# Optimization experiments

Hardware: AMD Instinct MI355X
Metric: run time of the kernel (lower is better)

## Reference

```python
import jax, jax.numpy as jnp
import numpy as np

ALPHA, BETA, GAMMA = 2.0, 2.0, 1.0
EPS = 1e-8  # torch F.cosine_similarity eps
B, T, D = 64, 1024, 256


def setup_inputs() -> dict:
    key = jax.random.key(0)
    k1, k2, k3 = jax.random.split(key, 3)
    f_v = jax.random.normal(k1, (B, T, D), dtype=jnp.float32)
    f_a = jax.random.normal(k2, (B, T, D), dtype=jnp.float32)
    labels = jax.random.randint(k3, (B,), 0, 2, dtype=jnp.int64)
    return {"f_v": f_v, "f_a": f_a, "labels": labels}


def _normalize(x):
    n = jnp.sqrt(jnp.sum(x * x, axis=-1, keepdims=True))
    return x / jnp.maximum(n, EPS)


def reference(f_v, f_a, labels):
    b, t, _ = f_v.shape
    vn = _normalize(f_v)  # [B,T,D]
    an = _normalize(f_a)  # [B,T,D]

    # --- per-timestep aligned-pair term ---
    cos_bt = jnp.sum(vn * an, axis=-1)  # [B,T] cosine sim
    d_bt = 1.0 - cos_bt                  # cosine distance
    pos_mask = (labels == 0).astype(f_v.dtype)[:, None]  # [B,1]
    neg_mask = 1.0 - pos_mask
    loss_pos = ALPHA * jnp.sum(d_bt * pos_mask)
    cnt_pos = jnp.sum(pos_mask) * t
    loss_neg = BETA * jnp.sum((1.0 - d_bt) * neg_mask)  # (1-d) == cos
    cnt_neg = jnp.sum(neg_mask) * t

    # --- cross-sample term: for i != j, (1 - mean_t d_ij) = mean_t cos(v_i_t, a_j_t) ---
    cross_cos = jnp.einsum('itd,jtd->ij', vn, an) / t  # [B,B] mean over T
    offdiag = 1.0 - jnp.eye(b, dtype=f_v.dtype)
    loss_neg = loss_neg + GAMMA * jnp.sum(cross_cos * offdiag)
    cnt_neg = cnt_neg + b * (b - 1)

    loss = jnp.where(cnt_pos > 0, loss_pos / jnp.maximum(cnt_pos, 1.0), 0.0)
    loss = loss + jnp.where(cnt_neg > 0, loss_neg / jnp.maximum(cnt_neg, 1.0), 0.0)
    return loss
```

## Files before the change

### kernel.cpp

```cpp
#include <hip/hip_runtime.h>

constexpr int Bn = 64;
constexpr int Tn = 1024;
constexpr int Dn = 256;

constexpr int TPB    = 256;
constexpr int NBLK   = 512;
constexpr int TPERB  = Tn / NBLK;
constexpr int KC     = 64;
constexpr int NCHUNK = Dn / KC;
constexpr int PITCH  = KC + 4;

__device__ __forceinline__ float dot4(const float4& a, const float4& b) {
    return a.x * b.x + a.y * b.y + a.z * b.z + a.w * b.w;
}

__global__ __launch_bounds__(TPB, 2)
void cmfm_main(const float* __restrict__ fv, const float* __restrict__ fa,
               const int* __restrict__ labels, float* __restrict__ acc) {
    __shared__ __align__(16) float Vs[Bn][PITCH];
    __shared__ __align__(16) float As[KC][PITCH];
    __shared__ float rvs[Bn];
    __shared__ float ras[Bn];
    __shared__ float wred[3][TPB / 64];

    const int tid = threadIdx.x;
    const int row = tid >> 2;
    const int q   = tid & 3;
    const int tx  = tid & 15;
    const int ty  = tid >> 4;
    const int i0  = ty * 4;
    const int j0  = tx * 4;

    const int lab = labels[row];

    const float4* __restrict__ fv4 = reinterpret_cast<const float4*>(fv);
    const float4* __restrict__ fa4 = reinterpret_cast<const float4*>(fa);

    float C[4][4] = {};
    float pos_acc = 0.f, neg_acc = 0.f;

    for (int tt = 0; tt < TPERB; ++tt) {
        const int t = blockIdx.x * TPERB + tt;
        const size_t base = ((size_t)row * Tn + t) * (Dn / 4);

        float S[4][4] = {};
        float sqv = 0.f, sqa = 0.f, dva = 0.f;

        for (int c = 0; c < NCHUNK; ++c) {
            const size_t f4base = base + (size_t)c * (KC / 4);
            float4 v4[4], a4[4];
            #pragma unroll
            for (int k = 0; k < 4; ++k) {
                const int f4i = q + 4 * k;
                v4[k] = fv4[f4base + f4i];
                a4[k] = fa4[f4base + f4i];
            }
            #pragma unroll
            for (int k = 0; k < 4; ++k) {
                sqv += dot4(v4[k], v4[k]);
                sqa += dot4(a4[k], a4[k]);
                dva += dot4(v4[k], a4[k]);
                const int d = (q + 4 * k) * 4;
                *reinterpret_cast<float4*>(&Vs[row][d]) = v4[k];
                As[d + 0][row] = a4[k].x;
                As[d + 1][row] = a4[k].y;
                As[d + 2][row] = a4[k].z;
                As[d + 3][row] = a4[k].w;
            }
            __syncthreads();

            #pragma unroll
            for (int d4 = 0; d4 < KC / 4; ++d4) {
                float va[4][4], ab[4][4];
                #pragma unroll
                for (int r = 0; r < 4; ++r) {
                    float4 v = *reinterpret_cast<const float4*>(&Vs[i0 + r][d4 * 4]);
                    va[r][0] = v.x; va[r][1] = v.y; va[r][2] = v.z; va[r][3] = v.w;
                }
                #pragma unroll
                for (int m = 0; m < 4; ++m) {
                    float4 a = *reinterpret_cast<const float4*>(&As[d4 * 4 + m][j0]);
                    ab[m][0] = a.x; ab[m][1] = a.y; ab[m][2] = a.z; ab[m][3] = a.w;
                }
                #pragma unroll
                for (int dd = 0; dd < 4; ++dd)
                    #pragma unroll
                    for (int r = 0; r < 4; ++r)
                        #pragma unroll
                        for (int s = 0; s < 4; ++s)
                            S[r][s] = fmaf(va[r][dd], ab[dd][s], S[r][s]);
            }
            __syncthreads();
        }

        sqv += __shfl_xor(sqv, 1); sqv += __shfl_xor(sqv, 2);
        sqa += __shfl_xor(sqa, 1); sqa += __shfl_xor(sqa, 2);
        dva += __shfl_xor(dva, 1); dva += __shfl_xor(dva, 2);
        const float rv = 1.f / fmaxf(sqrtf(sqv), 1e-8f);
        const float ra = 1.f / fmaxf(sqrtf(sqa), 1e-8f);
        if (q == 0) {
            rvs[row] = rv;
            ras[row] = ra;
            const float cosd = dva * rv * ra;
            if (lab == 0) pos_acc += 1.f - cosd;
            else          neg_acc += cosd;
        }
        __syncthreads();

        float rvv[4], raa[4];
        #pragma unroll
        for (int r = 0; r < 4; ++r) rvv[r] = rvs[i0 + r];
        #pragma unroll
        for (int s = 0; s < 4; ++s) raa[s] = ras[j0 + s];
        #pragma unroll
        for (int r = 0; r < 4; ++r)
            #pragma unroll
            for (int s = 0; s < 4; ++s)
                C[r][s] = fmaf(rvv[r] * raa[s], S[r][s], C[r][s]);
        __syncthreads();
    }

    float od = 0.f;
    #pragma unroll
    for (int r = 0; r < 4; ++r)
        #pragma unroll
        for (int s = 0; s < 4; ++s) od += C[r][s];
    if (ty == tx) {
        #pragma unroll
        for (int r = 0; r < 4; ++r) od -= C[r][r];
    }

    #pragma unroll
    for (int off = 1; off < 64; off <<= 1) {
        pos_acc += __shfl_xor(pos_acc, off);
        neg_acc += __shfl_xor(neg_acc, off);
        od      += __shfl_xor(od, off);
    }
    const int wave = tid >> 6;
    const int lane = tid & 63;
    if (lane == 0) {
        wred[0][wave] = pos_acc;
        wred[1][wave] = neg_acc;
        wred[2][wave] = od;
    }
    __syncthreads();
    if (tid == 0) {
        float p = 0.f, n = 0.f, o = 0.f;
        #pragma unroll
        for (int w = 0; w < TPB / 64; ++w) { p += wred[0][w]; n += wred[1][w]; o += wred[2][w]; }
        atomicAdd(&acc[0], p);
        atomicAdd(&acc[1], n);
        atomicAdd(&acc[2], o);
    }
}

__global__ void cmfm_final(const int* __restrict__ labels, const float* __restrict__ acc,
                           float* __restrict__ out) {
    if (threadIdx.x == 0) {
        int npos = 0;
        for (int i = 0; i < Bn; ++i) npos += (labels[i] == 0);
        const float pos_sum   = acc[0];
        const float neg_sum   = acc[1];
        const float cross_sum = acc[2];

        const float cnt_pos = (float)npos * (float)Tn;
        const float cnt_neg = (float)(Bn - npos) * (float)Tn + (float)Bn * (float)(Bn - 1);

        float loss = 0.f;
        if (npos > 0) loss += 2.0f * pos_sum / cnt_pos;
        loss += (2.0f * neg_sum + 1.0f * cross_sum / (float)Tn) / cnt_neg;
        out[0] = loss;
    }
}

extern "C" void kernel_launch(void* const* d_in, const int* in_sizes, int n_in,
                              void* d_out, int out_size, void* d_ws, size_t ws_size,
                              hipStream_t stream) {
    const float* fv     = (const float*)d_in[0];
    const float* fa     = (const float*)d_in[1];
    const int*   labels = (const int*)d_in[2];
    float* acc = (float*)d_ws;
    float* out = (float*)d_out;

    hipMemsetAsync(acc, 0, 3 * sizeof(float), stream);
    cmfm_main<<<NBLK, TPB, 0, stream>>>(fv, fa, labels, acc);
    cmfm_final<<<1, 64, 0, stream>>>(labels, acc, out);
}
```

Baseline: 171.0 us.

## Replace cross Gram matrix with sum-of-normalized-vectors dot product identity

Computes the off-diagonal cross-cosine sum as the dot of summed normalized v and a vectors per timestep minus the diagonal, eliminating the per-timestep 64x64 matrix product. Blocks now handle one timestep each and accumulate per-dimension column sums in shared memory over row groups. This turns a compute-bound kernel into a bandwidth-bound one, at the cost of possible float cancellation when subtracting the diagonal from the full sum.

```diff
diff --git a/kernel.cpp b/kernel.cpp
--- a/kernel.cpp
+++ b/kernel.cpp
@@ -4,154 +4,108 @@
 constexpr int Tn = 1024;
 constexpr int Dn = 256;
 
-constexpr int TPB    = 256;
-constexpr int NBLK   = 512;
-constexpr int TPERB  = Tn / NBLK;
-constexpr int KC     = 64;
-constexpr int NCHUNK = Dn / KC;
-constexpr int PITCH  = KC + 4;
+constexpr int TPB   = 256;
+constexpr int RG    = 16;
+constexpr int NG    = Bn / RG;
+constexpr int PITCH = Dn + 4;
 
 __device__ __forceinline__ float dot4(const float4& a, const float4& b) {
     return a.x * b.x + a.y * b.y + a.z * b.z + a.w * b.w;
 }
 
-__global__ __launch_bounds__(TPB, 2)
+__global__ __launch_bounds__(TPB, 4)
 void cmfm_main(const float* __restrict__ fv, const float* __restrict__ fa,
                const int* __restrict__ labels, float* __restrict__ acc) {
-    __shared__ __align__(16) float Vs[Bn][PITCH];
-    __shared__ __align__(16) float As[KC][PITCH];
-    __shared__ float rvs[Bn];
-    __shared__ float ras[Bn];
-    __shared__ float wred[3][TPB / 64];
+    __shared__ __align__(16) float Vs[RG][PITCH];
+    __shared__ __align__(16) float As[RG][PITCH];
+    __shared__ float rvl[RG];
+    __shared__ float ral[RG];
+    __shared__ float wred[4][TPB / 64];
 
     const int tid = threadIdx.x;
-    const int row = tid >> 2;
-    const int q   = tid & 3;
-    const int tx  = tid & 15;
-    const int ty  = tid >> 4;
-    const int i0  = ty * 4;
-    const int j0  = tx * 4;
-
-    const int lab = labels[row];
+    const int r16 = tid >> 4;
+    const int dp  = tid & 15;
+    const int t   = blockIdx.x;
 
     const float4* __restrict__ fv4 = reinterpret_cast<const float4*>(fv);
     const float4* __restrict__ fa4 = reinterpret_cast<const float4*>(fa);
 
-    float C[4][4] = {};
-    float pos_acc = 0.f, neg_acc = 0.f;
+    float pos_acc = 0.f, neg_acc = 0.f, diag_acc = 0.f;
+    float svd = 0.f, sad = 0.f;
 
-    for (int tt = 0; tt < TPERB; ++tt) {
-        const int t = blockIdx.x * TPERB + tt;
+    for (int g = 0; g < NG; ++g) {
+        const int row = g * RG + r16;
         const size_t base = ((size_t)row * Tn + t) * (Dn / 4);
 
-        float S[4][4] = {};
+        float4 v4[4], a4[4];
+        #pragma unroll
+        for (int k = 0; k < 4; ++k) {
+            v4[k] = fv4[base + dp + 16 * k];
+            a4[k] = fa4[base + dp + 16 * k];
+        }
         float sqv = 0.f, sqa = 0.f, dva = 0.f;
-
-        for (int c = 0; c < NCHUNK; ++c) {
-            const size_t f4base = base + (size_t)c * (KC / 4);
-            float4 v4[4], a4[4];
-            #pragma unroll
-            for (int k = 0; k < 4; ++k) {
-                const int f4i = q + 4 * k;
-                v4[k] = fv4[f4base + f4i];
-                a4[k] = fa4[f4base + f4i];
-            }
-            #pragma unroll
-            for (int k = 0; k < 4; ++k) {
-                sqv += dot4(v4[k], v4[k]);
-                sqa += dot4(a4[k], a4[k]);
-                dva += dot4(v4[k], a4[k]);
-                const int d = (q + 4 * k) * 4;
-                *reinterpret_cast<float4*>(&Vs[row][d]) = v4[k];
-                As[d + 0][row] = a4[k].x;
-                As[d + 1][row] = a4[k].y;
-                As[d + 2][row] = a4[k].z;
-                As[d + 3][row] = a4[k].w;
-            }
-            __syncthreads();
-
-            #pragma unroll
-            for (int d4 = 0; d4 < KC / 4; ++d4) {
-                float va[4][4], ab[4][4];
-                #pragma unroll
-                for (int r = 0; r < 4; ++r) {
-                    float4 v = *reinterpret_cast<const float4*>(&Vs[i0 + r][d4 * 4]);
-                    va[r][0] = v.x; va[r][1] = v.y; va[r][2] = v.z; va[r][3] = v.w;
-                }
-                #pragma unroll
-                for (int m = 0; m < 4; ++m) {
-                    float4 a = *reinterpret_cast<const float4*>(&As[d4 * 4 + m][j0]);
-                    ab[m][0] = a.x; ab[m][1] = a.y; ab[m][2] = a.z; ab[m][3] = a.w;
-                }
-                #pragma unroll
-                for (int dd = 0; dd < 4; ++dd)
-                    #pragma unroll
-                    for (int r = 0; r < 4; ++r)
-                        #pragma unroll
-                        for (int s = 0; s < 4; ++s)
-                            S[r][s] = fmaf(va[r][dd], ab[dd][s], S[r][s]);
-            }
-            __syncthreads();
+        #pragma unroll
+        for (int k = 0; k < 4; ++k) {
+            sqv += dot4(v4[k], v4[k]);
+            sqa += dot4(a4[k], a4[k]);
+            dva += dot4(v4[k], a4[k]);
+            const int d = (dp + 16 * k) * 4;
+            *reinterpret_cast<float4*>(&Vs[r16][d]) = v4[k];
+            *reinterpret_cast<float4*>(&As[r16][d]) = a4[k];
         }
-
-        sqv += __shfl_xor(sqv, 1); sqv += __shfl_xor(sqv, 2);
-        sqa += __shfl_xor(sqa, 1); sqa += __shfl_xor(sqa, 2);
-        dva += __shfl_xor(dva, 1); dva += __shfl_xor(dva, 2);
-        const float rv = 1.f / fmaxf(sqrtf(sqv), 1e-8f);
-        const float ra = 1.f / fmaxf(sqrtf(sqa), 1e-8f);
-        if (q == 0) {
-            rvs[row] = rv;
-            ras[row] = ra;
+        #pragma unroll
+        for (int off = 1; off < 16; off <<= 1) {
+            sqv += __shfl_xor(sqv, off);
+            sqa += __shfl_xor(sqa, off);
+            dva += __shfl_xor(dva, off);
+        }
+        if (dp == 0) {
+            const float rv = 1.f / fmaxf(sqrtf(sqv), 1e-8f);
+            const float ra = 1.f / fmaxf(sqrtf(sqa), 1e-8f);
+            rvl[r16] = rv;
+            ral[r16] = ra;
             const float cosd = dva * rv * ra;
-            if (lab == 0) pos_acc += 1.f - cosd;
-            else          neg_acc += cosd;
+            diag_acc += cosd;
+            if (labels[row] == 0) pos_acc += 1.f - cosd;
+            else                  neg_acc += cosd;
         }
         __syncthreads();
 
-        float rvv[4], raa[4];
         #pragma unroll
-        for (int r = 0; r < 4; ++r) rvv[r] = rvs[i0 + r];
-        #pragma unroll
-        for (int s = 0; s < 4; ++s) raa[s] = ras[j0 + s];
-        #pragma unroll
-        for (int r = 0; r < 4; ++r)
-            #pragma unroll
-            for (int s = 0; s < 4; ++s)
-                C[r][s] = fmaf(rvv[r] * raa[s], S[r][s], C[r][s]);
+        for (int i = 0; i < RG; ++i) {
+            svd = fmaf(rvl[i], Vs[i][tid], svd);
+            sad = fmaf(ral[i], As[i][tid], sad);
+        }
         __syncthreads();
     }
 
-    float od = 0.f;
-    #pragma unroll
-    for (int r = 0; r < 4; ++r)
-        #pragma unroll
-        for (int s = 0; s < 4; ++s) od += C[r][s];
-    if (ty == tx) {
-        #pragma unroll
-        for (int r = 0; r < 4; ++r) od -= C[r][r];
-    }
-
+    float dotp = svd * sad;
     #pragma unroll
     for (int off = 1; off < 64; off <<= 1) {
-        pos_acc += __shfl_xor(pos_acc, off);
-        neg_acc += __shfl_xor(neg_acc, off);
-        od      += __shfl_xor(od, off);
+        pos_acc  += __shfl_xor(pos_acc, off);
+        neg_acc  += __shfl_xor(neg_acc, off);
+        diag_acc += __shfl_xor(diag_acc, off);
+        dotp     += __shfl_xor(dotp, off);
     }
     const int wave = tid >> 6;
     const int lane = tid & 63;
     if (lane == 0) {
         wred[0][wave] = pos_acc;
         wred[1][wave] = neg_acc;
-        wred[2][wave] = od;
+        wred[2][wave] = dotp;
+        wred[3][wave] = diag_acc;
     }
     __syncthreads();
     if (tid == 0) {
-        float p = 0.f, n = 0.f, o = 0.f;
+        float p = 0.f, n = 0.f, o = 0.f, dg = 0.f;
         #pragma unroll
-        for (int w = 0; w < TPB / 64; ++w) { p += wred[0][w]; n += wred[1][w]; o += wred[2][w]; }
+        for (int w = 0; w < TPB / 64; ++w) {
+            p += wred[0][w]; n += wred[1][w]; o += wred[2][w]; dg += wred[3][w];
+        }
         atomicAdd(&acc[0], p);
         atomicAdd(&acc[1], n);
         atomicAdd(&acc[2], o);
+        atomicAdd(&acc[3], dg);
     }
 }
 
@@ -160,9 +114,11 @@
     if (threadIdx.x == 0) {
         int npos = 0;
         for (int i = 0; i < Bn; ++i) npos += (labels[i] == 0);
-        const float pos_sum   = acc[0];
-        const float neg_sum   = acc[1];
-        const float cross_sum = acc[2];
+        const float pos_sum  = acc[0];
+        const float neg_sum  = acc[1];
+        const float dot_sum  = acc[2];
+        const float diag_sum = acc[3];
+        const float cross_sum = dot_sum - diag_sum;
 
         const float cnt_pos = (float)npos * (float)Tn;
         const float cnt_neg = (float)(Bn - npos) * (float)Tn + (float)Bn * (float)(Bn - 1);
@@ -183,7 +139,7 @@
     float* acc = (float*)d_ws;
     float* out = (float*)d_out;
 
-    hipMemsetAsync(acc, 0, 3 * sizeof(float), stream);
-    cmfm_main<<<NBLK, TPB, 0, stream>>>(fv, fa, labels, acc);
+    hipMemsetAsync(acc, 0, 4 * sizeof(float), stream);
+    cmfm_main<<<Tn, TPB, 0, stream>>>(fv, fa, labels, acc);
     cmfm_final<<<1, 64, 0, stream>>>(labels, acc, out);
 }
```

Result: slower. 187.5 us (+9.6%).
